# Optimization experiments

Measured on AMD Instinct MI355X. Metric: run time of the kernel, lower is better.

Reference implementation:

```python
import jax, jax.numpy as jnp
import numpy as np

B, T, I, H = 64, 512, 256, 512


def setup_inputs() -> dict:
    key = jax.random.key(0)
    ks = jax.random.split(key, 3)
    x = jax.random.normal(ks[0], (B, T, I), dtype=jnp.float32)
    W = 0.1 * jax.random.normal(ks[1], (I, H), dtype=jnp.float32)
    U = 0.1 * jax.random.normal(ks[2], (H, H), dtype=jnp.float32)
    bias = jnp.ones((1, H), dtype=jnp.float32)
    alpha = jnp.full((1, 1), -3.0, dtype=jnp.float32)
    beta = jnp.full((1, 1), 3.0, dtype=jnp.float32)
    return {"x": x, "W": W, "U": U, "bias": bias, "alpha": alpha, "beta": beta}


def reference(x, W, U, bias, alpha, beta):
    # FastRNN: h_t = sigmoid(beta)*h_{t-1} + sigmoid(alpha)*tanh(W x_t + U h_{t-1} + b)
    sa = jax.nn.sigmoid(alpha)  # [1,1]
    sb = jax.nn.sigmoid(beta)   # [1,1]
    # Precompute input projection for all timesteps: [B,T,H]
    wx = jnp.einsum('bti,ih->bth', x, W)
    h0 = jnp.zeros((x.shape[0], U.shape[0]), dtype=x.dtype)

    def step(h, wx_t):
        pre = wx_t + h @ U + bias
        c = jnp.tanh(pre)
        h_new = sb * h + sa * c
        return h_new, h_new

    # scan over time: move T to leading axis
    _, hs = jax.lax.scan(step, h0, jnp.swapaxes(wx, 0, 1))
    return jnp.swapaxes(hs, 0, 1)  # [B,T,H]
```

## Files before the change

kernel.cpp:

```cpp
#include <hip/hip_runtime.h>
#include <stdint.h>


#define B_ 64
#define T_ 512
#define I_ 256
#define H_ 512
#define M_ (B_ * T_)

#define WXB_BYTES  ((size_t)M_ * H_ * 4)
#define HHALF_BYTES ((size_t)B_ * H_ * 2)

typedef short v8s __attribute__((ext_vector_type(8)));
typedef float v4f __attribute__((ext_vector_type(4)));
typedef unsigned long long u64t;

__device__ __forceinline__ uint16_t f2bf(float x) {
    union { float f; uint32_t u; } v; v.f = x;
    return (uint16_t)((v.u + 0x7FFFu + ((v.u >> 16) & 1u)) >> 16);
}

__global__ __launch_bounds__(256) void wx_gemm(
        const float* __restrict__ x, const float* __restrict__ W,
        const float* __restrict__ bias, float* __restrict__ wxb) {
    __shared__ uint16_t Asl[64][40];
    __shared__ uint16_t Bsl[4 * 64 * 8];

    const int tid = threadIdx.x;
    const int lane = tid & 63;
    const int w = tid >> 6;
    const int q = lane >> 4, c = lane & 15;
    const int mbase = (int)(blockIdx.x >> 3) * 64;
    const int nbase = (int)(blockIdx.x & 7) * 64;

    v4f acc[4];
    #pragma unroll
    for (int i = 0; i < 4; ++i) acc[i] = (v4f){0.f, 0.f, 0.f, 0.f};

    for (int ks = 0; ks < I_; ks += 32) {
        {
            int row = tid >> 2, c4 = tid & 3;
            const float* gp = x + (size_t)(mbase + row) * I_ + ks + c4 * 8;
            float4 f0 = *(const float4*)gp;
            float4 f1 = *(const float4*)(gp + 4);
            uint16_t* dp = &Asl[row][c4 * 8];
            dp[0] = f2bf(f0.x); dp[1] = f2bf(f0.y); dp[2] = f2bf(f0.z); dp[3] = f2bf(f0.w);
            dp[4] = f2bf(f1.x); dp[5] = f2bf(f1.y); dp[6] = f2bf(f1.z); dp[7] = f2bf(f1.w);
        }
        {
            int nt = tid >> 6;
            const float* gp = W + (size_t)(ks + q * 8) * H_ + nbase + nt * 16 + c;
            union { v8s v; uint16_t u[8]; } pk;
            #pragma unroll
            for (int jj = 0; jj < 8; ++jj) pk.u[jj] = f2bf(gp[(size_t)jj * H_]);
            *(v8s*)&Bsl[(nt * 64 + lane) * 8] = pk.v;
        }
        __syncthreads();
        const v8s* Bf = (const v8s*)Bsl;
        v8s a = *(const v8s*)&Asl[w * 16 + c][q * 8];
        #pragma unroll
        for (int nt = 0; nt < 4; ++nt) {
            v8s b = Bf[nt * 64 + lane];
            acc[nt] = __builtin_amdgcn_mfma_f32_16x16x32_bf16(a, b, acc[nt], 0, 0, 0);
        }
        __syncthreads();
    }
    #pragma unroll
    for (int nt = 0; nt < 4; ++nt) {
        int j = nbase + nt * 16 + c;
        float bj = bias[j];
        #pragma unroll
        for (int r = 0; r < 4; ++r) {
            int m = mbase + w * 16 + q * 4 + r;
            wxb[(size_t)m * H_ + j] = acc[nt][r] + bj;
        }
    }
}

__global__ __launch_bounds__(256, 1) void rnn_scan(
        const float* __restrict__ U, const float* __restrict__ wxb,
        const float* __restrict__ alpha, const float* __restrict__ beta,
        float* __restrict__ out, uint16_t* __restrict__ Hbuf) {
    __shared__ __align__(16) uint16_t Als[2][16][520];

    const int bid = blockIdx.x;
    const int g = bid >> 2, s = bid & 3;
    const int tid = threadIdx.x;
    const int lane = tid & 63;
    const int w = tid >> 6;
    const int q = lane >> 4, c = lane & 15;

    float sa, sb;
    { float a = alpha[0], b = beta[0];
      sa = 1.f / (1.f + __expf(-a)); sb = 1.f / (1.f + __expf(-b)); }

    v8s Uf[2][16];
    #pragma unroll
    for (int nt = 0; nt < 2; ++nt) {
        int jg = s * 128 + (2 * w + nt) * 16 + c;
        #pragma unroll
        for (int slot = 0; slot < 16; ++slot) {
            int ktile = (slot < 12) ? (slot + ((slot >= (s << 2)) ? 4 : 0))
                                    : ((s << 2) + slot - 12);
            const float* gp = U + (size_t)(ktile * 32 + q * 8) * H_ + jg;
            union { v8s v; uint16_t u[8]; } pk;
            #pragma unroll
            for (int jj = 0; jj < 8; ++jj) pk.u[jj] = f2bf(gp[(size_t)jj * H_]);
            Uf[nt][slot] = pk.v;
        }
    }
    float hold[2][4];
    #pragma unroll
    for (int nt = 0; nt < 2; ++nt)
        #pragma unroll
        for (int r = 0; r < 4; ++r) hold[nt][r] = 0.f;

    float wxv[2][4], wxn[2][4];
    #pragma unroll
    for (int nt = 0; nt < 2; ++nt) {
        int jg = s * 128 + (2 * w + nt) * 16 + c;
        #pragma unroll
        for (int r = 0; r < 4; ++r) {
            int bg = g * 16 + q * 4 + r;
            wxn[nt][r] = __builtin_nontemporal_load(
                &wxb[((size_t)bg * T_ + 0) * H_ + jg]);
        }
    }

    const int prow = tid >> 4;
    size_t poffv[3];
    int pcolv[3];
    #pragma unroll
    for (int i = 0; i < 3; ++i) {
        int sp = i + ((i >= s) ? 1 : 0);
        pcolv[i] = sp * 128 + (tid & 15) * 8;
        poffv[i] = ((size_t)(g * 16 + prow)) * H_ + pcolv[i];
    }
    const int orow = tid >> 4;
    const int ocol = s * 128 + (tid & 15) * 8;
    const size_t ooff = ((size_t)(g * 16 + orow)) * H_ + ocol;

    #pragma unroll
    for (int u = 0; u < 8; ++u)
        *((u64t*)&Als[0][tid >> 4][0] + (tid & 15) * 8 + u) = 0;

    u64t ev[3][2];
    v4f accO0 = (v4f){0.f, 0.f, 0.f, 0.f};
    v4f accO1 = (v4f){0.f, 0.f, 0.f, 0.f};

    for (int t = 0; t < T_; ++t) {
        const int p = t & 1;

        if (t > 0) {
            const uint16_t* hbp = Hbuf + (size_t)p * (B_ * H_);
            const u64t lsb = 0x0001000100010001ull;
            const u64t want = ((t >> 1) & 1) ? lsb : 0ull;
            for (int guard = 0; guard < (1 << 20); ++guard) {
                u64t x = (ev[0][0] ^ want) | (ev[0][1] ^ want)
                       | (ev[1][0] ^ want) | (ev[1][1] ^ want)
                       | (ev[2][0] ^ want) | (ev[2][1] ^ want);
                if (!(x & lsb)) break;
                #pragma unroll
                for (int i = 0; i < 3; ++i) {
                    const u64t* gp = (const u64t*)(hbp + poffv[i]);
                    ev[i][0] = __hip_atomic_load(&gp[0], __ATOMIC_RELAXED,
                                                 __HIP_MEMORY_SCOPE_AGENT);
                    ev[i][1] = __hip_atomic_load(&gp[1], __ATOMIC_RELAXED,
                                                 __HIP_MEMORY_SCOPE_AGENT);
                }
            }
            #pragma unroll
            for (int i = 0; i < 3; ++i) {
                u64t* dp = (u64t*)&Als[p][prow][pcolv[i]];
                dp[0] = ev[i][0]; dp[1] = ev[i][1];
            }
        }
        __syncthreads();
        v4f acc0 = accO0;
        v4f acc1 = accO1;
        #pragma unroll
        for (int i = 0; i < 12; ++i) {
            int ktp = i + ((i >= (s << 2)) ? 4 : 0);
            v8s a = *(const v8s*)((const uint16_t*)&Als[p][c][0] + ktp * 32 + q * 8);
            acc0 = __builtin_amdgcn_mfma_f32_16x16x32_bf16(a, Uf[0][i], acc0, 0, 0, 0);
            acc1 = __builtin_amdgcn_mfma_f32_16x16x32_bf16(a, Uf[1][i], acc1, 0, 0, 0);
        }
        #pragma unroll
        for (int nt = 0; nt < 2; ++nt)
            #pragma unroll
            for (int r = 0; r < 4; ++r) wxv[nt][r] = wxn[nt][r];
        const uint16_t tauw = (uint16_t)(((t + 1) >> 1) & 1);
        #pragma unroll
        for (int nt = 0; nt < 2; ++nt) {
            v4f av = nt ? acc1 : acc0;
            int jl = s * 128 + (2 * w + nt) * 16 + c;
            #pragma unroll
            for (int r = 0; r < 4; ++r) {
                float pre = av[r] + wxv[nt][r];
                float ex = __expf(pre + pre);
                float ct = 1.f - 2.f * __builtin_amdgcn_rcpf(ex + 1.f);
                float hn = sb * hold[nt][r] + sa * ct;
                hold[nt][r] = hn;
                Als[1 - p][q * 4 + r][jl] = (uint16_t)((f2bf(hn) & 0xFFFEu) | tauw);
            }
        }
        __syncthreads();
        if (t + 1 < T_) {
            {
                const u64t* sp = (const u64t*)&Als[1 - p][orow][ocol];
                u64t o0 = sp[0], o1 = sp[1];
                u64t* pp = (u64t*)(Hbuf + (size_t)(1 - p) * (B_ * H_) + ooff);
                __hip_atomic_store(&pp[0], o0, __ATOMIC_RELAXED,
                                   __HIP_MEMORY_SCOPE_AGENT);
                __hip_atomic_store(&pp[1], o1, __ATOMIC_RELAXED,
                                   __HIP_MEMORY_SCOPE_AGENT);
            }
            accO0 = (v4f){0.f, 0.f, 0.f, 0.f};
            accO1 = (v4f){0.f, 0.f, 0.f, 0.f};
            #pragma unroll
            for (int i = 0; i < 4; ++i) {
                int kto = (s << 2) + i;
                v8s a = *(const v8s*)((const uint16_t*)&Als[1 - p][c][0] + kto * 32 + q * 8);
                accO0 = __builtin_amdgcn_mfma_f32_16x16x32_bf16(a, Uf[0][12 + i], accO0, 0, 0, 0);
                accO1 = __builtin_amdgcn_mfma_f32_16x16x32_bf16(a, Uf[1][12 + i], accO1, 0, 0, 0);
            }
            const uint16_t* hbn = Hbuf + (size_t)(1 - p) * (B_ * H_);
            #pragma unroll
            for (int i = 0; i < 3; ++i) {
                const u64t* gp = (const u64t*)(hbn + poffv[i]);
                ev[i][0] = __hip_atomic_load(&gp[0], __ATOMIC_RELAXED,
                                             __HIP_MEMORY_SCOPE_AGENT);
                ev[i][1] = __hip_atomic_load(&gp[1], __ATOMIC_RELAXED,
                                             __HIP_MEMORY_SCOPE_AGENT);
            }
            #pragma unroll
            for (int nt = 0; nt < 2; ++nt) {
                int jg = s * 128 + (2 * w + nt) * 16 + c;
                #pragma unroll
                for (int r = 0; r < 4; ++r) {
                    int bg = g * 16 + q * 4 + r;
                    wxn[nt][r] = __builtin_nontemporal_load(
                        &wxb[((size_t)bg * T_ + (t + 1)) * H_ + jg]);
                }
            }
        }
        #pragma unroll
        for (int nt = 0; nt < 2; ++nt) {
            int jg = s * 128 + (2 * w + nt) * 16 + c;
            #pragma unroll
            for (int r = 0; r < 4; ++r) {
                int bg = g * 16 + q * 4 + r;
                out[((size_t)bg * T_ + t) * H_ + jg] = hold[nt][r];
            }
        }
    }
}

extern "C" void kernel_launch(void* const* d_in, const int* in_sizes, int n_in,
                              void* d_out, int out_size, void* d_ws, size_t ws_size,
                              hipStream_t stream) {
    const float* x     = (const float*)d_in[0];
    const float* W     = (const float*)d_in[1];
    const float* U     = (const float*)d_in[2];
    const float* bias  = (const float*)d_in[3];
    const float* alpha = (const float*)d_in[4];
    const float* beta  = (const float*)d_in[5];
    float* out = (float*)d_out;

    char* ws = (char*)d_ws;
    float* wxb = (float*)ws;
    uint16_t* Hbuf = (uint16_t*)(ws + WXB_BYTES);

    hipMemsetAsync(Hbuf, 0x00, HHALF_BYTES, stream);
    hipMemsetAsync((char*)Hbuf + HHALF_BYTES, 0xFF, HHALF_BYTES, stream);

    wx_gemm<<<dim3((M_ / 64) * (H_ / 64)), dim3(256), 0, stream>>>(x, W, bias, wxb);
    rnn_scan<<<dim3(16), dim3(256), 0, stream>>>(U, wxb, alpha, beta, out, Hbuf);
}
```

Baseline: 1.203 ms.

## Fuse input projection GEMM into the recurrent scan kernel

Removes the separate wx_gemm kernel and its 64 MB fp32 intermediate buffer. Each scan block now keeps its slice of W in registers as bf16 fragments and computes W·x_t with MFMA at every step, using x rows staged through double-buffered LDS and prefetched one step ahead. This drops a kernel launch plus the intermediate write and re-read, but adds 16 MFMAs and extra register pressure to the latency-critical serial step, and runs on only 16 blocks.

```diff
diff --git a/kernel.cpp b/kernel.cpp
--- a/kernel.cpp
+++ b/kernel.cpp
@@ -6,9 +6,7 @@
 #define T_ 512
 #define I_ 256
 #define H_ 512
-#define M_ (B_ * T_)
-
-#define WXB_BYTES  ((size_t)M_ * H_ * 4)
+
 #define HHALF_BYTES ((size_t)B_ * H_ * 2)
 
 typedef short v8s __attribute__((ext_vector_type(8)));
@@ -20,68 +18,13 @@
     return (uint16_t)((v.u + 0x7FFFu + ((v.u >> 16) & 1u)) >> 16);
 }
 
-__global__ __launch_bounds__(256) void wx_gemm(
+__global__ __launch_bounds__(256, 1) void rnn_scan(
         const float* __restrict__ x, const float* __restrict__ W,
-        const float* __restrict__ bias, float* __restrict__ wxb) {
-    __shared__ uint16_t Asl[64][40];
-    __shared__ uint16_t Bsl[4 * 64 * 8];
-
-    const int tid = threadIdx.x;
-    const int lane = tid & 63;
-    const int w = tid >> 6;
-    const int q = lane >> 4, c = lane & 15;
-    const int mbase = (int)(blockIdx.x >> 3) * 64;
-    const int nbase = (int)(blockIdx.x & 7) * 64;
-
-    v4f acc[4];
-    #pragma unroll
-    for (int i = 0; i < 4; ++i) acc[i] = (v4f){0.f, 0.f, 0.f, 0.f};
-
-    for (int ks = 0; ks < I_; ks += 32) {
-        {
-            int row = tid >> 2, c4 = tid & 3;
-            const float* gp = x + (size_t)(mbase + row) * I_ + ks + c4 * 8;
-            float4 f0 = *(const float4*)gp;
-            float4 f1 = *(const float4*)(gp + 4);
-            uint16_t* dp = &Asl[row][c4 * 8];
-            dp[0] = f2bf(f0.x); dp[1] = f2bf(f0.y); dp[2] = f2bf(f0.z); dp[3] = f2bf(f0.w);
-            dp[4] = f2bf(f1.x); dp[5] = f2bf(f1.y); dp[6] = f2bf(f1.z); dp[7] = f2bf(f1.w);
-        }
-        {
-            int nt = tid >> 6;
-            const float* gp = W + (size_t)(ks + q * 8) * H_ + nbase + nt * 16 + c;
-            union { v8s v; uint16_t u[8]; } pk;
-            #pragma unroll
-            for (int jj = 0; jj < 8; ++jj) pk.u[jj] = f2bf(gp[(size_t)jj * H_]);
-            *(v8s*)&Bsl[(nt * 64 + lane) * 8] = pk.v;
-        }
-        __syncthreads();
-        const v8s* Bf = (const v8s*)Bsl;
-        v8s a = *(const v8s*)&Asl[w * 16 + c][q * 8];
-        #pragma unroll
-        for (int nt = 0; nt < 4; ++nt) {
-            v8s b = Bf[nt * 64 + lane];
-            acc[nt] = __builtin_amdgcn_mfma_f32_16x16x32_bf16(a, b, acc[nt], 0, 0, 0);
-        }
-        __syncthreads();
-    }
-    #pragma unroll
-    for (int nt = 0; nt < 4; ++nt) {
-        int j = nbase + nt * 16 + c;
-        float bj = bias[j];
-        #pragma unroll
-        for (int r = 0; r < 4; ++r) {
-            int m = mbase + w * 16 + q * 4 + r;
-            wxb[(size_t)m * H_ + j] = acc[nt][r] + bj;
-        }
-    }
-}
-
-__global__ __launch_bounds__(256, 1) void rnn_scan(
-        const float* __restrict__ U, const float* __restrict__ wxb,
+        const float* __restrict__ U, const float* __restrict__ bias,
         const float* __restrict__ alpha, const float* __restrict__ beta,
         float* __restrict__ out, uint16_t* __restrict__ Hbuf) {
     __shared__ __align__(16) uint16_t Als[2][16][520];
+    __shared__ __align__(16) uint16_t xls[2][16][264];
 
     const int bid = blockIdx.x;
     const int g = bid >> 2, s = bid & 3;
@@ -109,23 +52,29 @@
             Uf[nt][slot] = pk.v;
         }
     }
-    float hold[2][4];
-    #pragma unroll
-    for (int nt = 0; nt < 2; ++nt)
-        #pragma unroll
-        for (int r = 0; r < 4; ++r) hold[nt][r] = 0.f;
-
-    float wxv[2][4], wxn[2][4];
+    v8s Wf[2][8];
     #pragma unroll
     for (int nt = 0; nt < 2; ++nt) {
         int jg = s * 128 + (2 * w + nt) * 16 + c;
         #pragma unroll
-        for (int r = 0; r < 4; ++r) {
-            int bg = g * 16 + q * 4 + r;
-            wxn[nt][r] = __builtin_nontemporal_load(
-                &wxb[((size_t)bg * T_ + 0) * H_ + jg]);
-        }
-    }
+        for (int kt = 0; kt < 8; ++kt) {
+            const float* gp = W + (size_t)(kt * 32 + q * 8) * H_ + jg;
+            union { v8s v; uint16_t u[8]; } pk;
+            #pragma unroll
+            for (int jj = 0; jj < 8; ++jj) pk.u[jj] = f2bf(gp[(size_t)jj * H_]);
+            Wf[nt][kt] = pk.v;
+        }
+    }
+    float bias_r[2];
+    #pragma unroll
+    for (int nt = 0; nt < 2; ++nt)
+        bias_r[nt] = bias[s * 128 + (2 * w + nt) * 16 + c];
+
+    float hold[2][4];
+    #pragma unroll
+    for (int nt = 0; nt < 2; ++nt)
+        #pragma unroll
+        for (int r = 0; r < 4; ++r) hold[nt][r] = 0.f;
 
     const int prow = tid >> 4;
     size_t poffv[3];
@@ -144,22 +93,54 @@
     for (int u = 0; u < 8; ++u)
         *((u64t*)&Als[0][tid >> 4][0] + (tid & 15) * 8 + u) = 0;
 
+    const int r0 = tid >> 4, c16 = (tid & 15) * 16;
+    {
+        const float* gx = x + ((size_t)(g * 16 + r0) * T_ + 0) * I_ + c16;
+        float4 f0 = *(const float4*)(gx + 0);
+        float4 f1 = *(const float4*)(gx + 4);
+        float4 f2 = *(const float4*)(gx + 8);
+        float4 f3 = *(const float4*)(gx + 12);
+        uint16_t* dp = &xls[0][r0][c16];
+        dp[0] = f2bf(f0.x); dp[1] = f2bf(f0.y); dp[2]  = f2bf(f0.z); dp[3]  = f2bf(f0.w);
+        dp[4] = f2bf(f1.x); dp[5] = f2bf(f1.y); dp[6]  = f2bf(f1.z); dp[7]  = f2bf(f1.w);
+        dp[8] = f2bf(f2.x); dp[9] = f2bf(f2.y); dp[10] = f2bf(f2.z); dp[11] = f2bf(f2.w);
+        dp[12] = f2bf(f3.x); dp[13] = f2bf(f3.y); dp[14] = f2bf(f3.z); dp[15] = f2bf(f3.w);
+    }
+    const float* xptr = x + ((size_t)(g * 16 + r0) * T_ + 1) * I_ + c16;
+    float4 xr0 = *(const float4*)(xptr + 0);
+    float4 xr1 = *(const float4*)(xptr + 4);
+    float4 xr2 = *(const float4*)(xptr + 8);
+    float4 xr3 = *(const float4*)(xptr + 12);
+    xptr += I_;
+
     u64t ev[3][2];
     v4f accO0 = (v4f){0.f, 0.f, 0.f, 0.f};
     v4f accO1 = (v4f){0.f, 0.f, 0.f, 0.f};
 
+    __syncthreads();
+
     for (int t = 0; t < T_; ++t) {
         const int p = t & 1;
+
+        v4f accX0 = (v4f){0.f, 0.f, 0.f, 0.f};
+        v4f accX1 = (v4f){0.f, 0.f, 0.f, 0.f};
+        #pragma unroll
+        for (int kt = 0; kt < 8; ++kt) {
+            v8s a = *(const v8s*)((const uint16_t*)&xls[p][c][0] + kt * 32 + q * 8);
+            accX0 = __builtin_amdgcn_mfma_f32_16x16x32_bf16(a, Wf[0][kt], accX0, 0, 0, 0);
+            accX1 = __builtin_amdgcn_mfma_f32_16x16x32_bf16(a, Wf[1][kt], accX1, 0, 0, 0);
+        }
+        __builtin_amdgcn_sched_barrier(0);
 
         if (t > 0) {
             const uint16_t* hbp = Hbuf + (size_t)p * (B_ * H_);
             const u64t lsb = 0x0001000100010001ull;
             const u64t want = ((t >> 1) & 1) ? lsb : 0ull;
             for (int guard = 0; guard < (1 << 20); ++guard) {
-                u64t x = (ev[0][0] ^ want) | (ev[0][1] ^ want)
-                       | (ev[1][0] ^ want) | (ev[1][1] ^ want)
-                       | (ev[2][0] ^ want) | (ev[2][1] ^ want);
-                if (!(x & lsb)) break;
+                u64t xx = (ev[0][0] ^ want) | (ev[0][1] ^ want)
+                        | (ev[1][0] ^ want) | (ev[1][1] ^ want)
+                        | (ev[2][0] ^ want) | (ev[2][1] ^ want);
+                if (!(xx & lsb)) break;
                 #pragma unroll
                 for (int i = 0; i < 3; ++i) {
                     const u64t* gp = (const u64t*)(hbp + poffv[i]);
@@ -176,8 +157,8 @@
             }
         }
         __syncthreads();
-        v4f acc0 = accO0;
-        v4f acc1 = accO1;
+        v4f acc0 = accO0 + accX0;
+        v4f acc1 = accO1 + accX1;
         #pragma unroll
         for (int i = 0; i < 12; ++i) {
             int ktp = i + ((i >= (s << 2)) ? 4 : 0);
@@ -185,10 +166,13 @@
             acc0 = __builtin_amdgcn_mfma_f32_16x16x32_bf16(a, Uf[0][i], acc0, 0, 0, 0);
             acc1 = __builtin_amdgcn_mfma_f32_16x16x32_bf16(a, Uf[1][i], acc1, 0, 0, 0);
         }
-        #pragma unroll
-        for (int nt = 0; nt < 2; ++nt)
-            #pragma unroll
-            for (int r = 0; r < 4; ++r) wxv[nt][r] = wxn[nt][r];
+        if (t + 1 < T_) {
+            uint16_t* dp = &xls[1 - p][r0][c16];
+            dp[0] = f2bf(xr0.x); dp[1] = f2bf(xr0.y); dp[2]  = f2bf(xr0.z); dp[3]  = f2bf(xr0.w);
+            dp[4] = f2bf(xr1.x); dp[5] = f2bf(xr1.y); dp[6]  = f2bf(xr1.z); dp[7]  = f2bf(xr1.w);
+            dp[8] = f2bf(xr2.x); dp[9] = f2bf(xr2.y); dp[10] = f2bf(xr2.z); dp[11] = f2bf(xr2.w);
+            dp[12] = f2bf(xr3.x); dp[13] = f2bf(xr3.y); dp[14] = f2bf(xr3.z); dp[15] = f2bf(xr3.w);
+        }
         const uint16_t tauw = (uint16_t)(((t + 1) >> 1) & 1);
         #pragma unroll
         for (int nt = 0; nt < 2; ++nt) {
@@ -196,7 +180,7 @@
             int jl = s * 128 + (2 * w + nt) * 16 + c;
             #pragma unroll
             for (int r = 0; r < 4; ++r) {
-                float pre = av[r] + wxv[nt][r];
+                float pre = av[r] + bias_r[nt];
                 float ex = __expf(pre + pre);
                 float ct = 1.f - 2.f * __builtin_amdgcn_rcpf(ex + 1.f);
                 float hn = sb * hold[nt][r] + sa * ct;
@@ -233,15 +217,12 @@
                 ev[i][1] = __hip_atomic_load(&gp[1], __ATOMIC_RELAXED,
                                              __HIP_MEMORY_SCOPE_AGENT);
             }
-            #pragma unroll
-            for (int nt = 0; nt < 2; ++nt) {
-                int jg = s * 128 + (2 * w + nt) * 16 + c;
-                #pragma unroll
-                for (int r = 0; r < 4; ++r) {
-                    int bg = g * 16 + q * 4 + r;
-                    wxn[nt][r] = __builtin_nontemporal_load(
-                        &wxb[((size_t)bg * T_ + (t + 1)) * H_ + jg]);
-                }
+            if (t + 2 < T_) {
+                xr0 = *(const float4*)(xptr + 0);
+                xr1 = *(const float4*)(xptr + 4);
+                xr2 = *(const float4*)(xptr + 8);
+                xr3 = *(const float4*)(xptr + 12);
+                xptr += I_;
             }
         }
         #pragma unroll
@@ -267,13 +248,11 @@
     const float* beta  = (const float*)d_in[5];
     float* out = (float*)d_out;
 
-    char* ws = (char*)d_ws;
-    float* wxb = (float*)ws;
-    uint16_t* Hbuf = (uint16_t*)(ws + WXB_BYTES);
+    uint16_t* Hbuf = (uint16_t*)d_ws;
 
     hipMemsetAsync(Hbuf, 0x00, HHALF_BYTES, stream);
     hipMemsetAsync((char*)Hbuf + HHALF_BYTES, 0xFF, HHALF_BYTES, stream);
 
-    wx_gemm<<<dim3((M_ / 64) * (H_ / 64)), dim3(256), 0, stream>>>(x, W, bias, wxb);
-    rnn_scan<<<dim3(16), dim3(256), 0, stream>>>(U, wxb, alpha, beta, out, Hbuf);
+    rnn_scan<<<dim3(16), dim3(256), 0, stream>>>(
+        x, W, U, bias, alpha, beta, out, Hbuf);
 }
```

Result: slower. 1.440 ms (+19.7%).

## Fuse input-projection GEMM and recurrent scan into one kernel with per-element ready flags

Applied to the files above, without the earlier changes.

Merges the Wx GEMM and the scan into one launch. The first 16 blocks run the scan and the rest compute the GEMM, with tiles reordered so early timesteps finish first. Each GEMM output sets its low mantissa bit as a ready flag, and the scan spin-waits until all its values have the bit set, so the scan can start while the GEMM is still running. This adds a full memset of the 64 MB wxb buffer, slightly perturbs the wx values, and scan blocks must be resident before GEMM blocks or the spin-waits could deadlock.

```diff
diff --git a/kernel.cpp b/kernel.cpp
--- a/kernel.cpp
+++ b/kernel.cpp
@@ -7,6 +7,7 @@
 #define I_ 256
 #define H_ 512
 #define M_ (B_ * T_)
+#define NSCAN 16
 
 #define WXB_BYTES  ((size_t)M_ * H_ * 4)
 #define HHALF_BYTES ((size_t)B_ * H_ * 2)
@@ -20,75 +21,79 @@
     return (uint16_t)((v.u + 0x7FFFu + ((v.u >> 16) & 1u)) >> 16);
 }
 
-__global__ __launch_bounds__(256) void wx_gemm(
+__global__ __launch_bounds__(256, 1) void rnn_fused(
         const float* __restrict__ x, const float* __restrict__ W,
-        const float* __restrict__ bias, float* __restrict__ wxb) {
-    __shared__ uint16_t Asl[64][40];
-    __shared__ uint16_t Bsl[4 * 64 * 8];
+        const float* __restrict__ U, const float* __restrict__ bias,
+        const float* __restrict__ alpha, const float* __restrict__ beta,
+        float* __restrict__ out, float* __restrict__ wxb,
+        uint16_t* __restrict__ Hbuf) {
+    __shared__ __align__(16) uint16_t smem[41984];
 
     const int tid = threadIdx.x;
     const int lane = tid & 63;
     const int w = tid >> 6;
     const int q = lane >> 4, c = lane & 15;
-    const int mbase = (int)(blockIdx.x >> 3) * 64;
-    const int nbase = (int)(blockIdx.x & 7) * 64;
-
-    v4f acc[4];
-    #pragma unroll
-    for (int i = 0; i < 4; ++i) acc[i] = (v4f){0.f, 0.f, 0.f, 0.f};
-
-    for (int ks = 0; ks < I_; ks += 32) {
-        {
-            int row = tid >> 2, c4 = tid & 3;
-            const float* gp = x + (size_t)(mbase + row) * I_ + ks + c4 * 8;
-            float4 f0 = *(const float4*)gp;
-            float4 f1 = *(const float4*)(gp + 4);
-            uint16_t* dp = &Asl[row][c4 * 8];
-            dp[0] = f2bf(f0.x); dp[1] = f2bf(f0.y); dp[2] = f2bf(f0.z); dp[3] = f2bf(f0.w);
-            dp[4] = f2bf(f1.x); dp[5] = f2bf(f1.y); dp[6] = f2bf(f1.z); dp[7] = f2bf(f1.w);
-        }
-        {
-            int nt = tid >> 6;
-            const float* gp = W + (size_t)(ks + q * 8) * H_ + nbase + nt * 16 + c;
-            union { v8s v; uint16_t u[8]; } pk;
-            #pragma unroll
-            for (int jj = 0; jj < 8; ++jj) pk.u[jj] = f2bf(gp[(size_t)jj * H_]);
-            *(v8s*)&Bsl[(nt * 64 + lane) * 8] = pk.v;
-        }
-        __syncthreads();
-        const v8s* Bf = (const v8s*)Bsl;
-        v8s a = *(const v8s*)&Asl[w * 16 + c][q * 8];
+
+    if (blockIdx.x >= NSCAN) {
+        const int gbid = (int)blockIdx.x - NSCAN;
+        const int t0 = gbid >> 9, b = (gbid >> 3) & 63, n = gbid & 7;
+        const int mbase = b * T_ + t0 * 64;
+        const int nbase = n * 64;
+        uint16_t (*Asl)[40] = (uint16_t(*)[40])smem;
+        uint16_t* Bsl = smem + 64 * 40;
+
+        v4f acc[4];
+        #pragma unroll
+        for (int i = 0; i < 4; ++i) acc[i] = (v4f){0.f, 0.f, 0.f, 0.f};
+
+        for (int ks = 0; ks < I_; ks += 32) {
+            {
+                int row = tid >> 2, c4 = tid & 3;
+                const float* gp = x + (size_t)(mbase + row) * I_ + ks + c4 * 8;
+                float4 f0 = *(const float4*)gp;
+                float4 f1 = *(const float4*)(gp + 4);
+                uint16_t* dp = &Asl[row][c4 * 8];
+                dp[0] = f2bf(f0.x); dp[1] = f2bf(f0.y); dp[2] = f2bf(f0.z); dp[3] = f2bf(f0.w);
+                dp[4] = f2bf(f1.x); dp[5] = f2bf(f1.y); dp[6] = f2bf(f1.z); dp[7] = f2bf(f1.w);
+            }
+            {
+                int nt = tid >> 6;
+                const float* gp = W + (size_t)(ks + q * 8) * H_ + nbase + nt * 16 + c;
+                union { v8s v; uint16_t u[8]; } pk;
+                #pragma unroll
+                for (int jj = 0; jj < 8; ++jj) pk.u[jj] = f2bf(gp[(size_t)jj * H_]);
+                *(v8s*)&Bsl[(nt * 64 + lane) * 8] = pk.v;
+            }
+            __syncthreads();
+            const v8s* Bf = (const v8s*)Bsl;
+            v8s a = *(const v8s*)&Asl[w * 16 + c][q * 8];
+            #pragma unroll
+            for (int nt = 0; nt < 4; ++nt) {
+                v8s bfr = Bf[nt * 64 + lane];
+                acc[nt] = __builtin_amdgcn_mfma_f32_16x16x32_bf16(a, bfr, acc[nt], 0, 0, 0);
+            }
+            __syncthreads();
+        }
         #pragma unroll
         for (int nt = 0; nt < 4; ++nt) {
-            v8s b = Bf[nt * 64 + lane];
-            acc[nt] = __builtin_amdgcn_mfma_f32_16x16x32_bf16(a, b, acc[nt], 0, 0, 0);
-        }
-        __syncthreads();
-    }
-    #pragma unroll
-    for (int nt = 0; nt < 4; ++nt) {
-        int j = nbase + nt * 16 + c;
-        float bj = bias[j];
-        #pragma unroll
-        for (int r = 0; r < 4; ++r) {
-            int m = mbase + w * 16 + q * 4 + r;
-            wxb[(size_t)m * H_ + j] = acc[nt][r] + bj;
-        }
-    }
-}
-
-__global__ __launch_bounds__(256, 1) void rnn_scan(
-        const float* __restrict__ U, const float* __restrict__ wxb,
-        const float* __restrict__ alpha, const float* __restrict__ beta,
-        float* __restrict__ out, uint16_t* __restrict__ Hbuf) {
-    __shared__ __align__(16) uint16_t Als[2][16][520];
+            int j = nbase + nt * 16 + c;
+            float bj = bias[j];
+            #pragma unroll
+            for (int r = 0; r < 4; ++r) {
+                int m = mbase + w * 16 + q * 4 + r;
+                union { float f; uint32_t u; } v; v.f = acc[nt][r] + bj;
+                v.u |= 1u;
+                __hip_atomic_store((uint32_t*)&wxb[(size_t)m * H_ + j], v.u,
+                                   __ATOMIC_RELAXED, __HIP_MEMORY_SCOPE_AGENT);
+            }
+        }
+        return;
+    }
+
+    auto& Als = *(uint16_t(*)[2][16][520])smem;
 
     const int bid = blockIdx.x;
     const int g = bid >> 2, s = bid & 3;
-    const int tid = threadIdx.x;
-    const int lane = tid & 63;
-    const int w = tid >> 6;
-    const int q = lane >> 4, c = lane & 15;
 
     float sa, sb;
     { float a = alpha[0], b = beta[0];
@@ -122,8 +127,10 @@
         #pragma unroll
         for (int r = 0; r < 4; ++r) {
             int bg = g * 16 + q * 4 + r;
-            wxn[nt][r] = __builtin_nontemporal_load(
-                &wxb[((size_t)bg * T_ + 0) * H_ + jg]);
+            uint32_t u = __hip_atomic_load(
+                (const uint32_t*)&wxb[((size_t)bg * T_ + 0) * H_ + jg],
+                __ATOMIC_RELAXED, __HIP_MEMORY_SCOPE_AGENT);
+            wxn[nt][r] = __uint_as_float(u);
         }
     }
 
@@ -150,16 +157,20 @@
 
     for (int t = 0; t < T_; ++t) {
         const int p = t & 1;
+        #pragma unroll
+        for (int nt = 0; nt < 2; ++nt)
+            #pragma unroll
+            for (int r = 0; r < 4; ++r) wxv[nt][r] = wxn[nt][r];
 
         if (t > 0) {
             const uint16_t* hbp = Hbuf + (size_t)p * (B_ * H_);
             const u64t lsb = 0x0001000100010001ull;
             const u64t want = ((t >> 1) & 1) ? lsb : 0ull;
             for (int guard = 0; guard < (1 << 20); ++guard) {
-                u64t x = (ev[0][0] ^ want) | (ev[0][1] ^ want)
-                       | (ev[1][0] ^ want) | (ev[1][1] ^ want)
-                       | (ev[2][0] ^ want) | (ev[2][1] ^ want);
-                if (!(x & lsb)) break;
+                u64t xx = (ev[0][0] ^ want) | (ev[0][1] ^ want)
+                        | (ev[1][0] ^ want) | (ev[1][1] ^ want)
+                        | (ev[2][0] ^ want) | (ev[2][1] ^ want);
+                if (!(xx & lsb)) break;
                 #pragma unroll
                 for (int i = 0; i < 3; ++i) {
                     const u64t* gp = (const u64t*)(hbp + poffv[i]);
@@ -185,10 +196,29 @@
             acc0 = __builtin_amdgcn_mfma_f32_16x16x32_bf16(a, Uf[0][i], acc0, 0, 0, 0);
             acc1 = __builtin_amdgcn_mfma_f32_16x16x32_bf16(a, Uf[1][i], acc1, 0, 0, 0);
         }
-        #pragma unroll
-        for (int nt = 0; nt < 2; ++nt)
-            #pragma unroll
-            for (int r = 0; r < 4; ++r) wxv[nt][r] = wxn[nt][r];
+        {
+            for (int guard = 0; guard < (1 << 20); ++guard) {
+                uint32_t andv = 0xFFFFFFFFu;
+                #pragma unroll
+                for (int nt = 0; nt < 2; ++nt)
+                    #pragma unroll
+                    for (int r = 0; r < 4; ++r)
+                        andv &= __float_as_uint(wxv[nt][r]);
+                if (andv & 1u) break;
+                #pragma unroll
+                for (int nt = 0; nt < 2; ++nt) {
+                    int jg = s * 128 + (2 * w + nt) * 16 + c;
+                    #pragma unroll
+                    for (int r = 0; r < 4; ++r) {
+                        int bg = g * 16 + q * 4 + r;
+                        uint32_t u = __hip_atomic_load(
+                            (const uint32_t*)&wxb[((size_t)bg * T_ + t) * H_ + jg],
+                            __ATOMIC_RELAXED, __HIP_MEMORY_SCOPE_AGENT);
+                        wxv[nt][r] = __uint_as_float(u);
+                    }
+                }
+            }
+        }
         const uint16_t tauw = (uint16_t)(((t + 1) >> 1) & 1);
         #pragma unroll
         for (int nt = 0; nt < 2; ++nt) {
@@ -224,6 +254,18 @@
                 accO0 = __builtin_amdgcn_mfma_f32_16x16x32_bf16(a, Uf[0][12 + i], accO0, 0, 0, 0);
                 accO1 = __builtin_amdgcn_mfma_f32_16x16x32_bf16(a, Uf[1][12 + i], accO1, 0, 0, 0);
             }
+            #pragma unroll
+            for (int nt = 0; nt < 2; ++nt) {
+                int jg = s * 128 + (2 * w + nt) * 16 + c;
+                #pragma unroll
+                for (int r = 0; r < 4; ++r) {
+                    int bg = g * 16 + q * 4 + r;
+                    uint32_t u = __hip_atomic_load(
+                        (const uint32_t*)&wxb[((size_t)bg * T_ + (t + 1)) * H_ + jg],
+                        __ATOMIC_RELAXED, __HIP_MEMORY_SCOPE_AGENT);
+                    wxn[nt][r] = __uint_as_float(u);
+                }
+            }
             const uint16_t* hbn = Hbuf + (size_t)(1 - p) * (B_ * H_);
             #pragma unroll
             for (int i = 0; i < 3; ++i) {
@@ -232,16 +274,6 @@
                                              __HIP_MEMORY_SCOPE_AGENT);
                 ev[i][1] = __hip_atomic_load(&gp[1], __ATOMIC_RELAXED,
                                              __HIP_MEMORY_SCOPE_AGENT);
-            }
-            #pragma unroll
-            for (int nt = 0; nt < 2; ++nt) {
-                int jg = s * 128 + (2 * w + nt) * 16 + c;
-                #pragma unroll
-                for (int r = 0; r < 4; ++r) {
-                    int bg = g * 16 + q * 4 + r;
-                    wxn[nt][r] = __builtin_nontemporal_load(
-                        &wxb[((size_t)bg * T_ + (t + 1)) * H_ + jg]);
-                }
             }
         }
         #pragma unroll
@@ -271,9 +303,10 @@
     float* wxb = (float*)ws;
     uint16_t* Hbuf = (uint16_t*)(ws + WXB_BYTES);
 
+    hipMemsetAsync(wxb, 0x00, WXB_BYTES, stream);
     hipMemsetAsync(Hbuf, 0x00, HHALF_BYTES, stream);
     hipMemsetAsync((char*)Hbuf + HHALF_BYTES, 0xFF, HHALF_BYTES, stream);
 
-    wx_gemm<<<dim3((M_ / 64) * (H_ / 64)), dim3(256), 0, stream>>>(x, W, bias, wxb);
-    rnn_scan<<<dim3(16), dim3(256), 0, stream>>>(U, wxb, alpha, beta, out, Hbuf);
+    rnn_fused<<<dim3(NSCAN + (M_ / 64) * (H_ / 64)), dim3(256), 0, stream>>>(
+        x, W, U, bias, alpha, beta, out, wxb, Hbuf);
 }
```

New measurement: 1.240 ms. 3.0% more time.

## Publish hidden state directly from registers in column-major exchange layout

Applied to the files above, without the earlier changes.

Changes the global hidden-state exchange buffer to a column-major-within-group layout, so each thread can pack its four computed bf16 values into one 64-bit word and store it straight from registers. This removes the LDS round trip and lets the global publish happen before the second __syncthreads, shortening the critical path between steps. On the read side, each 64-bit word is now unpacked into four scalar LDS writes, and the order of the wx prefetch and the polling loads is changed. The cost is more LDS store instructions and possible bank conflicts when unpacking.

```diff
diff --git a/kernel.cpp b/kernel.cpp
--- a/kernel.cpp
+++ b/kernel.cpp
@@ -10,6 +10,7 @@
 
 #define WXB_BYTES  ((size_t)M_ * H_ * 4)
 #define HHALF_BYTES ((size_t)B_ * H_ * 2)
+#define GSTRIDE (16 * H_)
 
 typedef short v8s __attribute__((ext_vector_type(8)));
 typedef float v4f __attribute__((ext_vector_type(4)));
@@ -127,18 +128,27 @@
         }
     }
 
-    const int prow = tid >> 4;
-    size_t poffv[3];
-    int pcolv[3];
+    size_t poff2[3][2];
+    int pcol2[3][2], prw2[3][2];
     #pragma unroll
     for (int i = 0; i < 3; ++i) {
         int sp = i + ((i >= s) ? 1 : 0);
-        pcolv[i] = sp * 128 + (tid & 15) * 8;
-        poffv[i] = ((size_t)(g * 16 + prow)) * H_ + pcolv[i];
-    }
-    const int orow = tid >> 4;
-    const int ocol = s * 128 + (tid & 15) * 8;
-    const size_t ooff = ((size_t)(g * 16 + orow)) * H_ + ocol;
+        #pragma unroll
+        for (int k = 0; k < 2; ++k) {
+            int u = tid * 2 + k;
+            int col = sp * 128 + (u >> 2);
+            int rq = u & 3;
+            pcol2[i][k] = col;
+            prw2[i][k] = rq * 4;
+            poff2[i][k] = (size_t)g * GSTRIDE + (size_t)col * 16 + rq * 4;
+        }
+    }
+    size_t ooff2[2];
+    #pragma unroll
+    for (int nt = 0; nt < 2; ++nt) {
+        int jl = s * 128 + (2 * w + nt) * 16 + c;
+        ooff2[nt] = (size_t)g * GSTRIDE + (size_t)jl * 16 + q * 4;
+    }
 
     #pragma unroll
     for (int u = 0; u < 8; ++u)
@@ -150,30 +160,39 @@
 
     for (int t = 0; t < T_; ++t) {
         const int p = t & 1;
+        #pragma unroll
+        for (int nt = 0; nt < 2; ++nt)
+            #pragma unroll
+            for (int r = 0; r < 4; ++r) wxv[nt][r] = wxn[nt][r];
 
         if (t > 0) {
             const uint16_t* hbp = Hbuf + (size_t)p * (B_ * H_);
             const u64t lsb = 0x0001000100010001ull;
             const u64t want = ((t >> 1) & 1) ? lsb : 0ull;
             for (int guard = 0; guard < (1 << 20); ++guard) {
-                u64t x = (ev[0][0] ^ want) | (ev[0][1] ^ want)
-                       | (ev[1][0] ^ want) | (ev[1][1] ^ want)
-                       | (ev[2][0] ^ want) | (ev[2][1] ^ want);
-                if (!(x & lsb)) break;
-                #pragma unroll
-                for (int i = 0; i < 3; ++i) {
-                    const u64t* gp = (const u64t*)(hbp + poffv[i]);
-                    ev[i][0] = __hip_atomic_load(&gp[0], __ATOMIC_RELAXED,
-                                                 __HIP_MEMORY_SCOPE_AGENT);
-                    ev[i][1] = __hip_atomic_load(&gp[1], __ATOMIC_RELAXED,
-                                                 __HIP_MEMORY_SCOPE_AGENT);
+                u64t xx = (ev[0][0] ^ want) | (ev[0][1] ^ want)
+                        | (ev[1][0] ^ want) | (ev[1][1] ^ want)
+                        | (ev[2][0] ^ want) | (ev[2][1] ^ want);
+                if (!(xx & lsb)) break;
+                #pragma unroll
+                for (int i = 0; i < 3; ++i)
+                    #pragma unroll
+                    for (int k = 0; k < 2; ++k)
+                        ev[i][k] = __hip_atomic_load(
+                            (const u64t*)(hbp + poff2[i][k]),
+                            __ATOMIC_RELAXED, __HIP_MEMORY_SCOPE_AGENT);
+            }
+            #pragma unroll
+            for (int i = 0; i < 3; ++i)
+                #pragma unroll
+                for (int k = 0; k < 2; ++k) {
+                    u64t v = ev[i][k];
+                    int col = pcol2[i][k], rw = prw2[i][k];
+                    Als[p][rw + 0][col] = (uint16_t)(v);
+                    Als[p][rw + 1][col] = (uint16_t)(v >> 16);
+                    Als[p][rw + 2][col] = (uint16_t)(v >> 32);
+                    Als[p][rw + 3][col] = (uint16_t)(v >> 48);
                 }
-            }
-            #pragma unroll
-            for (int i = 0; i < 3; ++i) {
-                u64t* dp = (u64t*)&Als[p][prow][pcolv[i]];
-                dp[0] = ev[i][0]; dp[1] = ev[i][1];
-            }
         }
         __syncthreads();
         v4f acc0 = accO0;
@@ -185,15 +204,13 @@
             acc0 = __builtin_amdgcn_mfma_f32_16x16x32_bf16(a, Uf[0][i], acc0, 0, 0, 0);
             acc1 = __builtin_amdgcn_mfma_f32_16x16x32_bf16(a, Uf[1][i], acc1, 0, 0, 0);
         }
-        #pragma unroll
-        for (int nt = 0; nt < 2; ++nt)
-            #pragma unroll
-            for (int r = 0; r < 4; ++r) wxv[nt][r] = wxn[nt][r];
         const uint16_t tauw = (uint16_t)(((t + 1) >> 1) & 1);
+        u64t pub[2];
         #pragma unroll
         for (int nt = 0; nt < 2; ++nt) {
             v4f av = nt ? acc1 : acc0;
             int jl = s * 128 + (2 * w + nt) * 16 + c;
+            u64t pk = 0;
             #pragma unroll
             for (int r = 0; r < 4; ++r) {
                 float pre = av[r] + wxv[nt][r];
@@ -201,20 +218,21 @@
                 float ct = 1.f - 2.f * __builtin_amdgcn_rcpf(ex + 1.f);
                 float hn = sb * hold[nt][r] + sa * ct;
                 hold[nt][r] = hn;
-                Als[1 - p][q * 4 + r][jl] = (uint16_t)((f2bf(hn) & 0xFFFEu) | tauw);
-            }
-        }
-        __syncthreads();
+                uint16_t tv = (uint16_t)((f2bf(hn) & 0xFFFEu) | tauw);
+                Als[1 - p][q * 4 + r][jl] = tv;
+                pk |= (u64t)tv << (16 * r);
+            }
+            pub[nt] = pk;
+        }
         if (t + 1 < T_) {
-            {
-                const u64t* sp = (const u64t*)&Als[1 - p][orow][ocol];
-                u64t o0 = sp[0], o1 = sp[1];
-                u64t* pp = (u64t*)(Hbuf + (size_t)(1 - p) * (B_ * H_) + ooff);
-                __hip_atomic_store(&pp[0], o0, __ATOMIC_RELAXED,
-                                   __HIP_MEMORY_SCOPE_AGENT);
-                __hip_atomic_store(&pp[1], o1, __ATOMIC_RELAXED,
-                                   __HIP_MEMORY_SCOPE_AGENT);
-            }
+            uint16_t* hb1 = Hbuf + (size_t)(1 - p) * (B_ * H_);
+            #pragma unroll
+            for (int nt = 0; nt < 2; ++nt)
+                __hip_atomic_store((u64t*)(hb1 + ooff2[nt]), pub[nt],
+                                   __ATOMIC_RELAXED, __HIP_MEMORY_SCOPE_AGENT);
+        }
+        __syncthreads();
+        if (t + 1 < T_) {
             accO0 = (v4f){0.f, 0.f, 0.f, 0.f};
             accO1 = (v4f){0.f, 0.f, 0.f, 0.f};
             #pragma unroll
@@ -224,15 +242,6 @@
                 accO0 = __builtin_amdgcn_mfma_f32_16x16x32_bf16(a, Uf[0][12 + i], accO0, 0, 0, 0);
                 accO1 = __builtin_amdgcn_mfma_f32_16x16x32_bf16(a, Uf[1][12 + i], accO1, 0, 0, 0);
             }
-            const uint16_t* hbn = Hbuf + (size_t)(1 - p) * (B_ * H_);
-            #pragma unroll
-            for (int i = 0; i < 3; ++i) {
-                const u64t* gp = (const u64t*)(hbn + poffv[i]);
-                ev[i][0] = __hip_atomic_load(&gp[0], __ATOMIC_RELAXED,
-                                             __HIP_MEMORY_SCOPE_AGENT);
-                ev[i][1] = __hip_atomic_load(&gp[1], __ATOMIC_RELAXED,
-                                             __HIP_MEMORY_SCOPE_AGENT);
-            }
             #pragma unroll
             for (int nt = 0; nt < 2; ++nt) {
                 int jg = s * 128 + (2 * w + nt) * 16 + c;
@@ -243,6 +252,14 @@
                         &wxb[((size_t)bg * T_ + (t + 1)) * H_ + jg]);
                 }
             }
+            const uint16_t* hbn = Hbuf + (size_t)(1 - p) * (B_ * H_);
+            #pragma unroll
+            for (int i = 0; i < 3; ++i)
+                #pragma unroll
+                for (int k = 0; k < 2; ++k)
+                    ev[i][k] = __hip_atomic_load(
+                        (const u64t*)(hbn + poff2[i][k]),
+                        __ATOMIC_RELAXED, __HIP_MEMORY_SCOPE_AGENT);
         }
         #pragma unroll
         for (int nt = 0; nt < 2; ++nt) {
```

New measurement: 1.140 ms. 5.3% less time.
